# Kernel optimization log

Measured on AMD Instinct MI355X. Metric: run time of the kernel, lower is better.

The kernel has to match this reference:

```python
import jax, jax.numpy as jnp
import numpy as np

B, N, M = 2, 4096, 4096
QUERY_DIM, CONTEXT_DIM = 512, 768
H, D = 8, 64
INNER = H * D


def setup_inputs() -> dict:
    key = jax.random.key(0)
    ks = jax.random.split(key, 8)
    x = jax.random.normal(ks[0], (B, N, QUERY_DIM), dtype=jnp.float32)
    context_tensor = jax.random.normal(ks[1], (B, M, CONTEXT_DIM), dtype=jnp.float32)
    mask = jax.random.randint(ks[2], (B, M), 0, 2) > 0  # bool [B, M]
    s = 0.02
    Wq = jax.random.normal(ks[3], (QUERY_DIM, INNER), dtype=jnp.float32) * s
    Wk = jax.random.normal(ks[4], (CONTEXT_DIM, INNER), dtype=jnp.float32) * s
    Wv = jax.random.normal(ks[5], (CONTEXT_DIM, INNER), dtype=jnp.float32) * s
    Wo = jax.random.normal(ks[6], (INNER, QUERY_DIM), dtype=jnp.float32) * s
    bo = jnp.zeros((QUERY_DIM,), dtype=jnp.float32)
    return {"x": x, "context_tensor": context_tensor, "mask": mask,
            "Wq": Wq, "Wk": Wk, "Wv": Wv, "Wo": Wo, "bo": bo}


def reference(x, context_tensor, mask, Wq, Wk, Wv, Wo, bo):
    scale = D ** (-0.5)
    # projections -> [B, T, H, D]
    q = (x @ Wq).reshape(B, N, H, D)
    k = (context_tensor @ Wk).reshape(B, M, H, D)
    v = (context_tensor @ Wv).reshape(B, M, H, D)
    # scores [B, H, N, M]
    attn = jnp.einsum('bnhd,bmhd->bhnm', q, k) * scale
    neg = -jnp.finfo(attn.dtype).max
    attn = jnp.where(mask[:, None, None, :], attn, neg)
    attn = jax.nn.softmax(attn, axis=-1)
    out = jnp.einsum('bhnm,bmhd->bnhd', attn, v).reshape(B, N, INNER)
    return out @ Wo + bo  # dropout is 0.0 -> identity
```

## Files before the change

### kernel.cpp

```cpp
#include <hip/hip_runtime.h>

typedef unsigned short u16;
typedef unsigned int u32;
typedef __attribute__((ext_vector_type(8))) short bf16x8;
typedef __attribute__((ext_vector_type(4))) short bf16x4;
typedef __attribute__((ext_vector_type(4))) float f32x4;

#define CSC 0.1803368801111244f

__device__ __forceinline__ u16 f2b(float f) {
  union { float f; u32 u; } c; c.f = f;
  return (u16)((c.u + 0x8000u) >> 16);
}

__device__ __forceinline__ uint2 pk4(f32x4 p) {
  union { float f; u32 u; } c0, c1, c2, c3;
  c0.f = p[0]; c1.f = p[1]; c2.f = p[2]; c3.f = p[3];
  u32 a = c0.u + 0x8000u, b = c1.u + 0x8000u;
  u32 c = c2.u + 0x8000u, d = c3.u + 0x8000u;
  uint2 r;
  r.x = __builtin_amdgcn_perm(b, a, 0x07060302u);
  r.y = __builtin_amdgcn_perm(d, c, 0x07060302u);
  return r;
}

__device__ __forceinline__ bf16x4 pk4v(f32x4 p) {
  union { uint2 u; bf16x4 v; } c;
  c.u = pk4(p);
  return c.v;
}

__device__ __forceinline__ void async16(const void* g, void* s) {
  __builtin_amdgcn_global_load_lds(
      (const __attribute__((address_space(1))) u32*)g,
      (__attribute__((address_space(3))) u32*)s, 16, 0, 0);
}

__global__ void prep(const float* __restrict__ x, const float* __restrict__ ctx,
                     const int* __restrict__ mask,
                     const float* __restrict__ Wq, const float* __restrict__ Wk,
                     const float* __restrict__ Wv, const float* __restrict__ Wo,
                     u16* __restrict__ Xb, u16* __restrict__ Cb,
                     float* __restrict__ mvalid, float* __restrict__ cnt,
                     u16* __restrict__ Wtq, u16* __restrict__ Wtkv, u16* __restrict__ Wto) {
  __shared__ u16 Tl[64 * 65];
  __shared__ int cred[4];
  const int bid = blockIdx.x, tid = threadIdx.x;
  if (bid < 10240) {
    const float* src; u16* dst; int i;
    if (bid < 4096) { i = (bid * 256 + tid) * 4; src = x; dst = Xb; }
    else { i = ((bid - 4096) * 256 + tid) * 4; src = ctx; dst = Cb; }
    float4 f = *(const float4*)&src[i];
    ushort4 o;
    o.x = f2b(f.x); o.y = f2b(f.y); o.z = f2b(f.z); o.w = f2b(f.w);
    *(ushort4*)&dst[i] = o;
  } else if (bid < 10560) {
    int t = bid - 10240;
    const float* W; u16* Wt; int Kd, tt;
    if (t < 64)       { W = Wq; Wt = Wtq;  Kd = 512; tt = t; }
    else if (t < 160) { W = Wk; Wt = Wtkv; Kd = 768; tt = t - 64; }
    else if (t < 256) { W = Wv; Wt = Wtkv + (size_t)512 * 768; Kd = 768; tt = t - 160; }
    else              { W = Wo; Wt = Wto;  Kd = 512; tt = t - 256; }
    const int k0 = (tt >> 3) * 64, n0 = (tt & 7) * 64;
    {
      const int r = tid >> 2, cg = (tid & 3) * 16;
#pragma unroll
      for (int i = 0; i < 4; i++) {
        float4 f = *(const float4*)&W[(size_t)(k0 + r) * 512 + n0 + cg + i * 4];
        Tl[r * 65 + cg + i * 4 + 0] = f2b(f.x);
        Tl[r * 65 + cg + i * 4 + 1] = f2b(f.y);
        Tl[r * 65 + cg + i * 4 + 2] = f2b(f.z);
        Tl[r * 65 + cg + i * 4 + 3] = f2b(f.w);
      }
    }
    __syncthreads();
    {
      const int n = tid >> 2, kg = (tid & 3) * 16;
      u16 buf[16];
#pragma unroll
      for (int i = 0; i < 16; i++) buf[i] = Tl[(kg + i) * 65 + n];
      u16* dst = &Wt[(size_t)(n0 + n) * Kd + k0 + kg];
      *(uint4*)dst = *(const uint4*)&buf[0];
      *(uint4*)(dst + 8) = *(const uint4*)&buf[8];
    }
  } else {
    const int b = bid - 10560;
    const int base = b * 4096;
    const int w = tid >> 6, lane = tid & 63;
    int zc = 0;
#pragma unroll
    for (int j = 0; j < 16; j++) {
      int idx = tid + j * 256;
      int mv = mask[base + idx];
      mvalid[base + idx] = mv ? 1.f : 0.f;
      zc += (mv == 0);
    }
#pragma unroll
    for (int d = 1; d < 64; d <<= 1) zc += __shfl_xor(zc, d);
    if (lane == 0) cred[w] = zc;
    __syncthreads();
    if (tid == 0) cnt[b] = (float)(cred[0] + cred[1] + cred[2] + cred[3]);
  }
}

__global__ __launch_bounds__(256, 6)
void gemm_qkv(const u16* __restrict__ Xb, const u16* __restrict__ Cb,
              const u16* __restrict__ Wtq, const u16* __restrict__ Wtkv,
              const float* __restrict__ mvalid,
              u16* __restrict__ Qb, u16* __restrict__ Kb, u16* __restrict__ Vt) {
  __shared__ u16 As[64 * 64];
  __shared__ u16 Bs[128 * 64];
  const int tid = threadIdx.x;
  const int w = tid >> 6, lane = tid & 63, quad = lane >> 4, l16 = lane & 15;
  const int wr = w >> 1, wc = w & 1;
  const int y = blockIdx.y;
  const bool isQ = (y < 4);
  const u16* A  = isQ ? Xb : Cb;
  const u16* Bt = isQ ? Wtq : Wtkv;
  const int K   = isQ ? 512 : 768;
  const int n0  = isQ ? y * 128 : (y - 4) * 128;
  const size_t m0 = (size_t)blockIdx.x * 64;
  const u16* Ab = A + m0 * K;
  const u16* Bb = Bt + (size_t)n0 * K;

  const int cswz = (((lane & 7) ^ ((lane >> 3) & 7)) << 3);
  const int sw0 = ((quad ^ (l16 & 7)) << 3);
  const int sw1 = sw0 ^ 32;
  const int r8 = lane >> 3;

  f32x4 acc[2][4];
#pragma unroll
  for (int i = 0; i < 2; i++)
#pragma unroll
    for (int j = 0; j < 4; j++) acc[i][j] = (f32x4){0.f, 0.f, 0.f, 0.f};

  for (int k0 = 0; k0 < K; k0 += 64) {
    async16(Ab + (size_t)(w * 16 + r8) * K + k0 + cswz, &As[(w * 16) * 64]);
    async16(Ab + (size_t)(w * 16 + 8 + r8) * K + k0 + cswz, &As[(w * 16 + 8) * 64]);
#pragma unroll
    for (int t = 0; t < 4; t++)
      async16(Bb + (size_t)(w * 32 + t * 8 + r8) * K + k0 + cswz, &Bs[(w * 32 + t * 8) * 64]);
    __syncthreads();
#pragma unroll
    for (int ks = 0; ks < 2; ks++) {
      const int so = ks ? sw1 : sw0;
      bf16x8 af[2], bfr[4];
#pragma unroll
      for (int i = 0; i < 2; i++)
        af[i] = *(const bf16x8*)&As[(wr * 32 + i * 16 + l16) * 64 + so];
#pragma unroll
      for (int j = 0; j < 4; j++)
        bfr[j] = *(const bf16x8*)&Bs[(wc * 64 + j * 16 + l16) * 64 + so];
#pragma unroll
      for (int i = 0; i < 2; i++)
#pragma unroll
        for (int j = 0; j < 4; j++)
          acc[i][j] = __builtin_amdgcn_mfma_f32_16x16x32_bf16(af[i], bfr[j], acc[i][j], 0, 0, 0);
    }
    __syncthreads();
  }

  if (isQ) {
#pragma unroll
    for (int i = 0; i < 2; i++)
#pragma unroll
      for (int j = 0; j < 4; j++)
#pragma unroll
        for (int r = 0; r < 4; r++) {
          size_t row = m0 + wr * 32 + i * 16 + quad * 4 + r;
          Qb[row * 512 + n0 + wc * 64 + j * 16 + l16] = f2b(acc[i][j][r]);
        }
  } else if (n0 < 512) {
#pragma unroll
    for (int i = 0; i < 2; i++) {
      size_t row0 = m0 + wr * 32 + i * 16 + quad * 4;
      f32x4 vm = *(const f32x4*)&mvalid[row0];
#pragma unroll
      for (int j = 0; j < 4; j++)
#pragma unroll
        for (int r = 0; r < 4; r++)
          Kb[(row0 + r) * 512 + n0 + wc * 64 + j * 16 + l16] = f2b(acc[i][j][r] * (vm[r] * CSC));
    }
  } else {
#pragma unroll
    for (int i = 0; i < 2; i++) {
      size_t row0 = m0 + wr * 32 + i * 16 + quad * 4;
      f32x4 vm = *(const f32x4*)&mvalid[row0];
#pragma unroll
      for (int j = 0; j < 4; j++) {
        int d = n0 - 512 + wc * 64 + j * 16 + l16;
        f32x4 v;
#pragma unroll
        for (int r = 0; r < 4; r++) v[r] = acc[i][j][r] * vm[r];
        *(uint2*)&Vt[(size_t)d * 8192 + row0] = pk4(v);
      }
    }
  }
}

__global__ __launch_bounds__(256, 4)
void gemm_o(const u16* __restrict__ A, const u16* __restrict__ Bt,
            const float* __restrict__ bias, float* __restrict__ Cf) {
  __shared__ u16 As[64 * 64];
  __shared__ u16 Bs[64 * 64];
  const int tid = threadIdx.x;
  const int w = tid >> 6, lane = tid & 63, quad = lane >> 4, l16 = lane & 15;
  const size_t m0 = (size_t)blockIdx.x * 64;
  const int n0 = blockIdx.y * 64;
  const u16* Ab = A + m0 * 512;
  const u16* Bb = Bt + (size_t)n0 * 512;

  const int cswz = (((lane & 7) ^ ((lane >> 3) & 7)) << 3);
  const int sw0 = ((quad ^ (l16 & 7)) << 3);
  const int sw1 = sw0 ^ 32;
  const int r8 = lane >> 3;

  f32x4 acc[4];
#pragma unroll
  for (int j = 0; j < 4; j++) acc[j] = (f32x4){0.f, 0.f, 0.f, 0.f};

  for (int k0 = 0; k0 < 512; k0 += 64) {
    async16(Ab + (size_t)(w * 16 + r8) * 512 + k0 + cswz, &As[(w * 16) * 64]);
    async16(Ab + (size_t)(w * 16 + 8 + r8) * 512 + k0 + cswz, &As[(w * 16 + 8) * 64]);
    async16(Bb + (size_t)(w * 16 + r8) * 512 + k0 + cswz, &Bs[(w * 16) * 64]);
    async16(Bb + (size_t)(w * 16 + 8 + r8) * 512 + k0 + cswz, &Bs[(w * 16 + 8) * 64]);
    __syncthreads();
#pragma unroll
    for (int ks = 0; ks < 2; ks++) {
      const int so = ks ? sw1 : sw0;
      bf16x8 af = *(const bf16x8*)&As[(w * 16 + l16) * 64 + so];
#pragma unroll
      for (int j = 0; j < 4; j++) {
        bf16x8 bfr = *(const bf16x8*)&Bs[(j * 16 + l16) * 64 + so];
        acc[j] = __builtin_amdgcn_mfma_f32_16x16x32_bf16(af, bfr, acc[j], 0, 0, 0);
      }
    }
    __syncthreads();
  }

#pragma unroll
  for (int j = 0; j < 4; j++)
#pragma unroll
    for (int r = 0; r < 4; r++) {
      size_t row = m0 + w * 16 + quad * 4 + r;
      int col = n0 + j * 16 + l16;
      Cf[row * 512 + col] = acc[j][r] + bias[col];
    }
}

__global__ __launch_bounds__(256, 4)
void attn_kernel(const u16* __restrict__ Q, const u16* __restrict__ Kg,
                 const u16* __restrict__ Vt, const float* __restrict__ cnt,
                 u16* __restrict__ AO) {
  __shared__ u16 Ks[2][64 * 64];
  __shared__ u16 Vs[2][64 * 64];

  const int tid = threadIdx.x;
  const int w = tid >> 6, lane = tid & 63, quad = lane >> 4, l16 = lane & 15;
  const int l = blockIdx.x;
  const int qb = l >> 4, hb = l & 15, h = hb >> 1, b = hb & 1;
  const size_t qrow0 = (size_t)b * 4096 + (size_t)qb * 64;
  const size_t crow0 = (size_t)b * 4096;
  const int hcol = h * 64;
  const float cb = cnt[b];

  const int cswz = (((lane & 7) ^ ((lane >> 3) & 7)) << 3);
  const int sw0 = ((quad ^ (l16 & 7)) << 3);
  const int sw1 = sw0 ^ 32;
  const int r8 = lane >> 3;

  bf16x8 qf[2];
#pragma unroll
  for (int ks = 0; ks < 2; ks++)
    qf[ks] = *(const bf16x8*)&Q[(qrow0 + w * 16 + l16) * 512 + hcol + ks * 32 + quad * 8];

  async16(Kg + (crow0 + w * 16 + r8) * 512 + hcol + cswz, &Ks[0][(w * 16) * 64]);
  async16(Kg + (crow0 + w * 16 + 8 + r8) * 512 + hcol + cswz, &Ks[0][(w * 16 + 8) * 64]);
  async16(Vt + (size_t)(hcol + w * 16 + r8) * 8192 + crow0 + cswz, &Vs[0][(w * 16) * 64]);
  async16(Vt + (size_t)(hcol + w * 16 + 8 + r8) * 8192 + crow0 + cswz, &Vs[0][(w * 16 + 8) * 64]);
  __syncthreads();

  f32x4 Oacc[4];
#pragma unroll
  for (int dt = 0; dt < 4; dt++) Oacc[dt] = (f32x4){0.f, 0.f, 0.f, 0.f};
  float lsum = 0.f;

  for (int mt = 0; mt < 64; mt++) {
    const int cur = mt & 1;
    const size_t m0 = (size_t)mt * 64;

    if (mt < 63) {
      const size_t mn = m0 + 64;
      async16(Kg + (crow0 + mn + w * 16 + r8) * 512 + hcol + cswz, &Ks[cur ^ 1][(w * 16) * 64]);
      async16(Kg + (crow0 + mn + w * 16 + 8 + r8) * 512 + hcol + cswz, &Ks[cur ^ 1][(w * 16 + 8) * 64]);
      async16(Vt + (size_t)(hcol + w * 16 + r8) * 8192 + crow0 + mn + cswz, &Vs[cur ^ 1][(w * 16) * 64]);
      async16(Vt + (size_t)(hcol + w * 16 + 8 + r8) * 8192 + crow0 + mn + cswz, &Vs[cur ^ 1][(w * 16 + 8) * 64]);
    }

    f32x4 sacc[4];
#pragma unroll
    for (int mtt = 0; mtt < 4; mtt++) sacc[mtt] = (f32x4){0.f, 0.f, 0.f, 0.f};
#pragma unroll
    for (int ks = 0; ks < 2; ks++) {
      const int so = ks ? sw1 : sw0;
#pragma unroll
      for (int mtt = 0; mtt < 4; mtt++) {
        bf16x8 kb = *(const bf16x8*)&Ks[cur][(mtt * 16 + l16) * 64 + so];
        sacc[mtt] = __builtin_amdgcn_mfma_f32_16x16x32_bf16(kb, qf[ks], sacc[mtt], 0, 0, 0);
      }
    }

    bf16x4 pf[4];
#pragma unroll
    for (int mtt = 0; mtt < 4; mtt++) {
      f32x4 p;
#pragma unroll
      for (int r = 0; r < 4; r++) {
        p[r] = __builtin_amdgcn_exp2f(sacc[mtt][r]);
        lsum += p[r];
      }
      pf[mtt] = pk4v(p);
    }

#pragma unroll
    for (int mtt = 0; mtt < 4; mtt++) {
#pragma unroll
      for (int dt = 0; dt < 4; dt++) {
        bf16x4 va = *(const bf16x4*)&Vs[cur][(dt * 16 + l16) * 64 +
                      (((mtt * 2 + (quad >> 1)) ^ (l16 & 7)) << 3) + ((quad & 1) << 2)];
        Oacc[dt] = __builtin_amdgcn_mfma_f32_16x16x16bf16_1k(va, pf[mtt], Oacc[dt], 0, 0, 0);
      }
    }
    __syncthreads();
  }

  lsum += __shfl_xor(lsum, 16);
  lsum += __shfl_xor(lsum, 32);
  const float inv = 1.0f / (lsum - cb);

#pragma unroll
  for (int dt = 0; dt < 4; dt++) {
    f32x4 o;
#pragma unroll
    for (int r = 0; r < 4; r++) o[r] = Oacc[dt][r] * inv;
    *(uint2*)&AO[(qrow0 + w * 16 + l16) * 512 + hcol + dt * 16 + quad * 4] = pk4(o);
  }
}


extern "C" void kernel_launch(void* const* d_in, const int* in_sizes, int n_in,
                              void* d_out, int out_size, void* d_ws, size_t ws_size,
                              hipStream_t stream) {
  const float* x   = (const float*)d_in[0];
  const float* ctx = (const float*)d_in[1];
  const int*  mask = (const int*)d_in[2];
  const float* Wq  = (const float*)d_in[3];
  const float* Wk  = (const float*)d_in[4];
  const float* Wv  = (const float*)d_in[5];
  const float* Wo  = (const float*)d_in[6];
  const float* bo  = (const float*)d_in[7];
  float* out = (float*)d_out;

  char* p = (char*)d_ws;
  u16* Xb   = (u16*)p; p += (size_t)8192 * 512 * 2;
  u16* Cb   = (u16*)p; p += (size_t)8192 * 768 * 2;
  u16* Wtq  = (u16*)p; p += (size_t)512 * 512 * 2;
  u16* Wtkv = (u16*)p; p += (size_t)1024 * 768 * 2;
  u16* Wto  = (u16*)p; p += (size_t)512 * 512 * 2;
  u16* Qb   = (u16*)p; p += (size_t)8192 * 512 * 2;
  u16* Kb   = (u16*)p; p += (size_t)8192 * 512 * 2;
  u16* Vtg  = (u16*)p; p += (size_t)512 * 8192 * 2;
  u16* AOb  = (u16*)p; p += (size_t)8192 * 512 * 2;
  float* mvalid = (float*)p; p += (size_t)8192 * 4;
  float* cnt    = (float*)p; p += 2 * 4;

  prep<<<10562, 256, 0, stream>>>(x, ctx, mask, Wq, Wk, Wv, Wo,
                                  Xb, Cb, mvalid, cnt, Wtq, Wtkv, Wto);
  gemm_qkv<<<dim3(128, 12), 256, 0, stream>>>(Xb, Cb, Wtq, Wtkv, mvalid, Qb, Kb, Vtg);
  attn_kernel<<<1024, 256, 0, stream>>>(Qb, Kb, Vtg, cnt, AOb);
  gemm_o<<<dim3(128, 8), 256, 0, stream>>>(AOb, Wto, bo, out);
}
```

Before: 226.3 us.

## Split attention work across waves by key tile instead of query rows

Each wave now handles all 64 query rows of the block but only a 16-key slice of every 64-key tile. Each wave loads one K fragment and one V fragment per tile and reuses them across four query tiles, cutting LDS reads per MFMA. The partial O accumulators and row sums are then combined through shared memory in a tree reduction at the end. The cost is four times as many accumulator registers, which is why the launch bound drops to 3 blocks per SIMD, plus extra syncs and LDS traffic in the epilogue.

```diff
diff --git a/kernel.cpp b/kernel.cpp
--- a/kernel.cpp
+++ b/kernel.cpp
@@ -248,12 +248,12 @@
     }
 }
 
-__global__ __launch_bounds__(256, 4)
+__global__ __launch_bounds__(256, 3)
 void attn_kernel(const u16* __restrict__ Q, const u16* __restrict__ Kg,
                  const u16* __restrict__ Vt, const float* __restrict__ cnt,
                  u16* __restrict__ AO) {
-  __shared__ u16 Ks[2][64 * 64];
-  __shared__ u16 Vs[2][64 * 64];
+  __shared__ u16 KV[4][64 * 64];
+  __shared__ float Lred[4][64];
 
   const int tid = threadIdx.x;
   const int w = tid >> 6, lane = tid & 63, quad = lane >> 4, l16 = lane & 15;
@@ -269,81 +269,135 @@
   const int sw1 = sw0 ^ 32;
   const int r8 = lane >> 3;
 
-  bf16x8 qf[2];
-#pragma unroll
-  for (int ks = 0; ks < 2; ks++)
-    qf[ks] = *(const bf16x8*)&Q[(qrow0 + w * 16 + l16) * 512 + hcol + ks * 32 + quad * 8];
-
-  async16(Kg + (crow0 + w * 16 + r8) * 512 + hcol + cswz, &Ks[0][(w * 16) * 64]);
-  async16(Kg + (crow0 + w * 16 + 8 + r8) * 512 + hcol + cswz, &Ks[0][(w * 16 + 8) * 64]);
-  async16(Vt + (size_t)(hcol + w * 16 + r8) * 8192 + crow0 + cswz, &Vs[0][(w * 16) * 64]);
-  async16(Vt + (size_t)(hcol + w * 16 + 8 + r8) * 8192 + crow0 + cswz, &Vs[0][(w * 16 + 8) * 64]);
+  bf16x8 qf[4][2];
+#pragma unroll
+  for (int qt = 0; qt < 4; qt++)
+#pragma unroll
+    for (int ks = 0; ks < 2; ks++)
+      qf[qt][ks] = *(const bf16x8*)&Q[(qrow0 + qt * 16 + l16) * 512 + hcol + ks * 32 + quad * 8];
+
+  async16(Kg + (crow0 + w * 16 + r8) * 512 + hcol + cswz, &KV[0][(w * 16) * 64]);
+  async16(Kg + (crow0 + w * 16 + 8 + r8) * 512 + hcol + cswz, &KV[0][(w * 16 + 8) * 64]);
+  async16(Vt + (size_t)(hcol + w * 16 + r8) * 8192 + crow0 + cswz, &KV[2][(w * 16) * 64]);
+  async16(Vt + (size_t)(hcol + w * 16 + 8 + r8) * 8192 + crow0 + cswz, &KV[2][(w * 16 + 8) * 64]);
   __syncthreads();
 
-  f32x4 Oacc[4];
-#pragma unroll
-  for (int dt = 0; dt < 4; dt++) Oacc[dt] = (f32x4){0.f, 0.f, 0.f, 0.f};
-  float lsum = 0.f;
+  f32x4 Oacc[4][4];
+#pragma unroll
+  for (int qt = 0; qt < 4; qt++)
+#pragma unroll
+    for (int dt = 0; dt < 4; dt++) Oacc[qt][dt] = (f32x4){0.f, 0.f, 0.f, 0.f};
+  float lsum[4] = {0.f, 0.f, 0.f, 0.f};
+
+  const int krow = (w * 16 + l16) * 64;
+  const int vbase = (((w * 2 + (quad >> 1)) ^ (l16 & 7)) << 3) + ((quad & 1) << 2);
 
   for (int mt = 0; mt < 64; mt++) {
     const int cur = mt & 1;
-    const size_t m0 = (size_t)mt * 64;
 
     if (mt < 63) {
-      const size_t mn = m0 + 64;
-      async16(Kg + (crow0 + mn + w * 16 + r8) * 512 + hcol + cswz, &Ks[cur ^ 1][(w * 16) * 64]);
-      async16(Kg + (crow0 + mn + w * 16 + 8 + r8) * 512 + hcol + cswz, &Ks[cur ^ 1][(w * 16 + 8) * 64]);
-      async16(Vt + (size_t)(hcol + w * 16 + r8) * 8192 + crow0 + mn + cswz, &Vs[cur ^ 1][(w * 16) * 64]);
-      async16(Vt + (size_t)(hcol + w * 16 + 8 + r8) * 8192 + crow0 + mn + cswz, &Vs[cur ^ 1][(w * 16 + 8) * 64]);
-    }
-
+      const size_t mn = (size_t)(mt + 1) * 64;
+      async16(Kg + (crow0 + mn + w * 16 + r8) * 512 + hcol + cswz, &KV[cur ^ 1][(w * 16) * 64]);
+      async16(Kg + (crow0 + mn + w * 16 + 8 + r8) * 512 + hcol + cswz, &KV[cur ^ 1][(w * 16 + 8) * 64]);
+      async16(Vt + (size_t)(hcol + w * 16 + r8) * 8192 + crow0 + mn + cswz, &KV[2 + (cur ^ 1)][(w * 16) * 64]);
+      async16(Vt + (size_t)(hcol + w * 16 + 8 + r8) * 8192 + crow0 + mn + cswz, &KV[2 + (cur ^ 1)][(w * 16 + 8) * 64]);
+    }
+
+    bf16x8 kf0 = *(const bf16x8*)&KV[cur][krow + sw0];
+    bf16x8 kf1 = *(const bf16x8*)&KV[cur][krow + sw1];
     f32x4 sacc[4];
 #pragma unroll
-    for (int mtt = 0; mtt < 4; mtt++) sacc[mtt] = (f32x4){0.f, 0.f, 0.f, 0.f};
-#pragma unroll
-    for (int ks = 0; ks < 2; ks++) {
-      const int so = ks ? sw1 : sw0;
-#pragma unroll
-      for (int mtt = 0; mtt < 4; mtt++) {
-        bf16x8 kb = *(const bf16x8*)&Ks[cur][(mtt * 16 + l16) * 64 + so];
-        sacc[mtt] = __builtin_amdgcn_mfma_f32_16x16x32_bf16(kb, qf[ks], sacc[mtt], 0, 0, 0);
+    for (int qt = 0; qt < 4; qt++) sacc[qt] = (f32x4){0.f, 0.f, 0.f, 0.f};
+#pragma unroll
+    for (int qt = 0; qt < 4; qt++)
+      sacc[qt] = __builtin_amdgcn_mfma_f32_16x16x32_bf16(kf0, qf[qt][0], sacc[qt], 0, 0, 0);
+#pragma unroll
+    for (int qt = 0; qt < 4; qt++)
+      sacc[qt] = __builtin_amdgcn_mfma_f32_16x16x32_bf16(kf1, qf[qt][1], sacc[qt], 0, 0, 0);
+
+    bf16x4 pf[4];
+#pragma unroll
+    for (int qt = 0; qt < 4; qt++) {
+      f32x4 p;
+#pragma unroll
+      for (int r = 0; r < 4; r++) {
+        p[r] = __builtin_amdgcn_exp2f(sacc[qt][r]);
+        lsum[qt] += p[r];
       }
-    }
-
-    bf16x4 pf[4];
-#pragma unroll
-    for (int mtt = 0; mtt < 4; mtt++) {
-      f32x4 p;
-#pragma unroll
-      for (int r = 0; r < 4; r++) {
-        p[r] = __builtin_amdgcn_exp2f(sacc[mtt][r]);
-        lsum += p[r];
+      pf[qt] = pk4v(p);
+    }
+
+#pragma unroll
+    for (int dt = 0; dt < 4; dt++) {
+      bf16x4 va = *(const bf16x4*)&KV[2 + cur][(dt * 16 + l16) * 64 + vbase];
+#pragma unroll
+      for (int qt = 0; qt < 4; qt++)
+        Oacc[qt][dt] = __builtin_amdgcn_mfma_f32_16x16x16bf16_1k(va, pf[qt], Oacc[qt][dt], 0, 0, 0);
+    }
+    __syncthreads();
+  }
+
+  float* Ored = (float*)&KV[0][0];
+
+#pragma unroll
+  for (int qt = 0; qt < 4; qt++) {
+    lsum[qt] += __shfl_xor(lsum[qt], 16);
+    lsum[qt] += __shfl_xor(lsum[qt], 32);
+  }
+  if (lane < 16) {
+#pragma unroll
+    for (int qt = 0; qt < 4; qt++) Lred[w][qt * 16 + l16] = lsum[qt];
+  }
+
+  if (w >= 2) {
+    float* dst = Ored + (w - 2) * 4096;
+#pragma unroll
+    for (int qt = 0; qt < 4; qt++)
+#pragma unroll
+      for (int dt = 0; dt < 4; dt++)
+#pragma unroll
+        for (int r = 0; r < 4; r++)
+          dst[(dt * 16 + quad * 4 + r) * 64 + qt * 16 + l16] = Oacc[qt][dt][r];
+  }
+  __syncthreads();
+  if (w < 2) {
+    const float* src = Ored + w * 4096;
+#pragma unroll
+    for (int qt = 0; qt < 4; qt++)
+#pragma unroll
+      for (int dt = 0; dt < 4; dt++)
+#pragma unroll
+        for (int r = 0; r < 4; r++)
+          Oacc[qt][dt][r] += src[(dt * 16 + quad * 4 + r) * 64 + qt * 16 + l16];
+  }
+  __syncthreads();
+  if (w == 1) {
+#pragma unroll
+    for (int qt = 0; qt < 4; qt++)
+#pragma unroll
+      for (int dt = 0; dt < 4; dt++)
+#pragma unroll
+        for (int r = 0; r < 4; r++)
+          Ored[(dt * 16 + quad * 4 + r) * 64 + qt * 16 + l16] = Oacc[qt][dt][r];
+  }
+  __syncthreads();
+  if (w == 0) {
+    float inv[4];
+#pragma unroll
+    for (int qt = 0; qt < 4; qt++) {
+      int q = qt * 16 + l16;
+      inv[qt] = 1.0f / (Lred[0][q] + Lred[1][q] + Lred[2][q] + Lred[3][q] - cb);
+    }
+#pragma unroll
+    for (int qt = 0; qt < 4; qt++)
+#pragma unroll
+      for (int dt = 0; dt < 4; dt++) {
+        f32x4 o;
+#pragma unroll
+        for (int r = 0; r < 4; r++)
+          o[r] = (Oacc[qt][dt][r] + Ored[(dt * 16 + quad * 4 + r) * 64 + qt * 16 + l16]) * inv[qt];
+        *(uint2*)&AO[(qrow0 + qt * 16 + l16) * 512 + hcol + dt * 16 + quad * 4] = pk4(o);
       }
-      pf[mtt] = pk4v(p);
-    }
-
-#pragma unroll
-    for (int mtt = 0; mtt < 4; mtt++) {
-#pragma unroll
-      for (int dt = 0; dt < 4; dt++) {
-        bf16x4 va = *(const bf16x4*)&Vs[cur][(dt * 16 + l16) * 64 +
-                      (((mtt * 2 + (quad >> 1)) ^ (l16 & 7)) << 3) + ((quad & 1) << 2)];
-        Oacc[dt] = __builtin_amdgcn_mfma_f32_16x16x16bf16_1k(va, pf[mtt], Oacc[dt], 0, 0, 0);
-      }
-    }
-    __syncthreads();
-  }
-
-  lsum += __shfl_xor(lsum, 16);
-  lsum += __shfl_xor(lsum, 32);
-  const float inv = 1.0f / (lsum - cb);
-
-#pragma unroll
-  for (int dt = 0; dt < 4; dt++) {
-    f32x4 o;
-#pragma unroll
-    for (int r = 0; r < 4; r++) o[r] = Oacc[dt][r] * inv;
-    *(uint2*)&AO[(qrow0 + w * 16 + l16) * 512 + hcol + dt * 16 + quad * 4] = pk4(o);
   }
 }
 
```

Result: slower. 238.7 us (+5.5%).

## Split attention KV range in halves, double query rows per warp, add combine kernel

Applied to the files above, without the earlier changes.

Each attention block now handles 128 query rows (32 per warp) and only half of the key/value sequence. Each K/V tile loaded into shared memory is therefore reused across twice as many queries, and the grid stays at 1024 blocks. Unnormalized fp32 partial outputs and row sums are written to a workspace, and a new combine kernel adds the two halves, normalizes and packs to bf16. This costs extra global traffic for the fp32 partials, one more launch, and higher register pressure from doubled accumulators.

```diff
diff --git a/kernel.cpp b/kernel.cpp
--- a/kernel.cpp
+++ b/kernel.cpp
@@ -250,29 +250,31 @@
 
 __global__ __launch_bounds__(256, 4)
 void attn_kernel(const u16* __restrict__ Q, const u16* __restrict__ Kg,
-                 const u16* __restrict__ Vt, const float* __restrict__ cnt,
-                 u16* __restrict__ AO) {
+                 const u16* __restrict__ Vt,
+                 float* __restrict__ Opart, float* __restrict__ Lpart) {
   __shared__ u16 Ks[2][64 * 64];
   __shared__ u16 Vs[2][64 * 64];
 
   const int tid = threadIdx.x;
   const int w = tid >> 6, lane = tid & 63, quad = lane >> 4, l16 = lane & 15;
   const int l = blockIdx.x;
-  const int qb = l >> 4, hb = l & 15, h = hb >> 1, b = hb & 1;
-  const size_t qrow0 = (size_t)b * 4096 + (size_t)qb * 64;
-  const size_t crow0 = (size_t)b * 4096;
+  const int hb = l & 15, half = (l >> 4) & 1, qb = l >> 5;
+  const int h = hb >> 1, b = hb & 1;
+  const size_t qrow0 = (size_t)b * 4096 + (size_t)qb * 128;
+  const size_t crow0 = (size_t)b * 4096 + (size_t)half * 2048;
   const int hcol = h * 64;
-  const float cb = cnt[b];
 
   const int cswz = (((lane & 7) ^ ((lane >> 3) & 7)) << 3);
   const int sw0 = ((quad ^ (l16 & 7)) << 3);
   const int sw1 = sw0 ^ 32;
   const int r8 = lane >> 3;
 
-  bf16x8 qf[2];
-#pragma unroll
-  for (int ks = 0; ks < 2; ks++)
-    qf[ks] = *(const bf16x8*)&Q[(qrow0 + w * 16 + l16) * 512 + hcol + ks * 32 + quad * 8];
+  bf16x8 qf[2][2];
+#pragma unroll
+  for (int qt = 0; qt < 2; qt++)
+#pragma unroll
+    for (int ks = 0; ks < 2; ks++)
+      qf[qt][ks] = *(const bf16x8*)&Q[(qrow0 + w * 32 + qt * 16 + l16) * 512 + hcol + ks * 32 + quad * 8];
 
   async16(Kg + (crow0 + w * 16 + r8) * 512 + hcol + cswz, &Ks[0][(w * 16) * 64]);
   async16(Kg + (crow0 + w * 16 + 8 + r8) * 512 + hcol + cswz, &Ks[0][(w * 16 + 8) * 64]);
@@ -280,71 +282,106 @@
   async16(Vt + (size_t)(hcol + w * 16 + 8 + r8) * 8192 + crow0 + cswz, &Vs[0][(w * 16 + 8) * 64]);
   __syncthreads();
 
-  f32x4 Oacc[4];
-#pragma unroll
-  for (int dt = 0; dt < 4; dt++) Oacc[dt] = (f32x4){0.f, 0.f, 0.f, 0.f};
-  float lsum = 0.f;
-
-  for (int mt = 0; mt < 64; mt++) {
+  f32x4 Oacc[2][4];
+#pragma unroll
+  for (int qt = 0; qt < 2; qt++)
+#pragma unroll
+    for (int dt = 0; dt < 4; dt++) Oacc[qt][dt] = (f32x4){0.f, 0.f, 0.f, 0.f};
+  float lsum[2] = {0.f, 0.f};
+
+  for (int mt = 0; mt < 32; mt++) {
     const int cur = mt & 1;
-    const size_t m0 = (size_t)mt * 64;
-
-    if (mt < 63) {
-      const size_t mn = m0 + 64;
-      async16(Kg + (crow0 + mn + w * 16 + r8) * 512 + hcol + cswz, &Ks[cur ^ 1][(w * 16) * 64]);
-      async16(Kg + (crow0 + mn + w * 16 + 8 + r8) * 512 + hcol + cswz, &Ks[cur ^ 1][(w * 16 + 8) * 64]);
-      async16(Vt + (size_t)(hcol + w * 16 + r8) * 8192 + crow0 + mn + cswz, &Vs[cur ^ 1][(w * 16) * 64]);
-      async16(Vt + (size_t)(hcol + w * 16 + 8 + r8) * 8192 + crow0 + mn + cswz, &Vs[cur ^ 1][(w * 16 + 8) * 64]);
-    }
-
-    f32x4 sacc[4];
-#pragma unroll
-    for (int mtt = 0; mtt < 4; mtt++) sacc[mtt] = (f32x4){0.f, 0.f, 0.f, 0.f};
+
+    if (mt < 31) {
+      const size_t mn = crow0 + (size_t)(mt + 1) * 64;
+      async16(Kg + (mn + w * 16 + r8) * 512 + hcol + cswz, &Ks[cur ^ 1][(w * 16) * 64]);
+      async16(Kg + (mn + w * 16 + 8 + r8) * 512 + hcol + cswz, &Ks[cur ^ 1][(w * 16 + 8) * 64]);
+      async16(Vt + (size_t)(hcol + w * 16 + r8) * 8192 + mn + cswz, &Vs[cur ^ 1][(w * 16) * 64]);
+      async16(Vt + (size_t)(hcol + w * 16 + 8 + r8) * 8192 + mn + cswz, &Vs[cur ^ 1][(w * 16 + 8) * 64]);
+    }
+
+    f32x4 sacc[2][4];
+#pragma unroll
+    for (int qt = 0; qt < 2; qt++)
+#pragma unroll
+      for (int mtt = 0; mtt < 4; mtt++) sacc[qt][mtt] = (f32x4){0.f, 0.f, 0.f, 0.f};
 #pragma unroll
     for (int ks = 0; ks < 2; ks++) {
       const int so = ks ? sw1 : sw0;
+      bf16x8 kb[4];
+#pragma unroll
+      for (int mtt = 0; mtt < 4; mtt++)
+        kb[mtt] = *(const bf16x8*)&Ks[cur][(mtt * 16 + l16) * 64 + so];
+#pragma unroll
+      for (int qt = 0; qt < 2; qt++)
+#pragma unroll
+        for (int mtt = 0; mtt < 4; mtt++)
+          sacc[qt][mtt] = __builtin_amdgcn_mfma_f32_16x16x32_bf16(kb[mtt], qf[qt][ks], sacc[qt][mtt], 0, 0, 0);
+    }
+
+    bf16x4 pf[2][4];
+#pragma unroll
+    for (int qt = 0; qt < 2; qt++) {
+      float rs = 0.f;
 #pragma unroll
       for (int mtt = 0; mtt < 4; mtt++) {
-        bf16x8 kb = *(const bf16x8*)&Ks[cur][(mtt * 16 + l16) * 64 + so];
-        sacc[mtt] = __builtin_amdgcn_mfma_f32_16x16x32_bf16(kb, qf[ks], sacc[mtt], 0, 0, 0);
+        f32x4 p;
+#pragma unroll
+        for (int r = 0; r < 4; r++) {
+          p[r] = __builtin_amdgcn_exp2f(sacc[qt][mtt][r]);
+          rs += p[r];
+        }
+        pf[qt][mtt] = pk4v(p);
       }
-    }
-
-    bf16x4 pf[4];
+      lsum[qt] += rs;
+    }
+
 #pragma unroll
     for (int mtt = 0; mtt < 4; mtt++) {
-      f32x4 p;
-#pragma unroll
-      for (int r = 0; r < 4; r++) {
-        p[r] = __builtin_amdgcn_exp2f(sacc[mtt][r]);
-        lsum += p[r];
-      }
-      pf[mtt] = pk4v(p);
-    }
-
-#pragma unroll
-    for (int mtt = 0; mtt < 4; mtt++) {
-#pragma unroll
-      for (int dt = 0; dt < 4; dt++) {
-        bf16x4 va = *(const bf16x4*)&Vs[cur][(dt * 16 + l16) * 64 +
+      bf16x4 va[4];
+#pragma unroll
+      for (int dt = 0; dt < 4; dt++)
+        va[dt] = *(const bf16x4*)&Vs[cur][(dt * 16 + l16) * 64 +
                       (((mtt * 2 + (quad >> 1)) ^ (l16 & 7)) << 3) + ((quad & 1) << 2)];
-        Oacc[dt] = __builtin_amdgcn_mfma_f32_16x16x16bf16_1k(va, pf[mtt], Oacc[dt], 0, 0, 0);
-      }
-    }
-    __syncthreads();
-  }
-
-  lsum += __shfl_xor(lsum, 16);
-  lsum += __shfl_xor(lsum, 32);
-  const float inv = 1.0f / (lsum - cb);
-
-#pragma unroll
-  for (int dt = 0; dt < 4; dt++) {
-    f32x4 o;
-#pragma unroll
-    for (int r = 0; r < 4; r++) o[r] = Oacc[dt][r] * inv;
-    *(uint2*)&AO[(qrow0 + w * 16 + l16) * 512 + hcol + dt * 16 + quad * 4] = pk4(o);
-  }
+#pragma unroll
+      for (int qt = 0; qt < 2; qt++)
+#pragma unroll
+        for (int dt = 0; dt < 4; dt++)
+          Oacc[qt][dt] = __builtin_amdgcn_mfma_f32_16x16x16bf16_1k(va[dt], pf[qt][mtt], Oacc[qt][dt], 0, 0, 0);
+    }
+    __syncthreads();
+  }
+
+#pragma unroll
+  for (int qt = 0; qt < 2; qt++) {
+    lsum[qt] += __shfl_xor(lsum[qt], 16);
+    lsum[qt] += __shfl_xor(lsum[qt], 32);
+    if (quad == 0)
+      Lpart[(size_t)half * 65536 + ((b * 8 + h) << 12) + qb * 128 + w * 32 + qt * 16 + l16] = lsum[qt];
+  }
+
+  float* Obuf = Opart + (size_t)half * 8192 * 512;
+#pragma unroll
+  for (int qt = 0; qt < 2; qt++)
+#pragma unroll
+    for (int dt = 0; dt < 4; dt++)
+      *(f32x4*)&Obuf[(qrow0 + w * 32 + qt * 16 + l16) * 512 + hcol + dt * 16 + quad * 4] = Oacc[qt][dt];
+}
+
+__global__ void combine(const float* __restrict__ Opart, const float* __restrict__ Lpart,
+                        const float* __restrict__ cnt, u16* __restrict__ AOb) {
+  const int idx = blockIdx.x * 256 + threadIdx.x;
+  const int row = idx >> 7, c4 = (idx & 127) << 2;
+  const int b = row >> 12, q = row & 4095, h = c4 >> 6;
+  const int li = ((b * 8 + h) << 12) + q;
+  const float inv = 1.0f / (Lpart[li] + Lpart[65536 + li] - cnt[b]);
+  const size_t off = (size_t)row * 512 + c4;
+  f32x4 o0 = *(const f32x4*)&Opart[off];
+  f32x4 o1 = *(const f32x4*)&Opart[(size_t)8192 * 512 + off];
+  f32x4 o;
+#pragma unroll
+  for (int r = 0; r < 4; r++) o[r] = (o0[r] + o1[r]) * inv;
+  *(uint2*)&AOb[off] = pk4(o);
 }
 
 
@@ -372,11 +409,14 @@
   u16* Vtg  = (u16*)p; p += (size_t)512 * 8192 * 2;
   u16* AOb  = (u16*)p; p += (size_t)8192 * 512 * 2;
   float* mvalid = (float*)p; p += (size_t)8192 * 4;
-  float* cnt    = (float*)p; p += 2 * 4;
+  float* cnt    = (float*)p; p += 256;
+  float* Opart  = (float*)p; p += (size_t)2 * 8192 * 512 * 4;
+  float* Lpart  = (float*)p; p += (size_t)2 * 65536 * 4;
 
   prep<<<10562, 256, 0, stream>>>(x, ctx, mask, Wq, Wk, Wv, Wo,
                                   Xb, Cb, mvalid, cnt, Wtq, Wtkv, Wto);
   gemm_qkv<<<dim3(128, 12), 256, 0, stream>>>(Xb, Cb, Wtq, Wtkv, mvalid, Qb, Kb, Vtg);
-  attn_kernel<<<1024, 256, 0, stream>>>(Qb, Kb, Vtg, cnt, AOb);
+  attn_kernel<<<1024, 256, 0, stream>>>(Qb, Kb, Vtg, Opart, Lpart);
+  combine<<<4096, 256, 0, stream>>>(Opart, Lpart, cnt, AOb);
   gemm_o<<<dim3(128, 8), 256, 0, stream>>>(AOb, Wto, bo, out);
 }
```

After: 244.7 us. 8.1% more time.
